# Performance work log

Measured on AMD Instinct MI355X. Metric: run time of the kernel, lower is better.

Reference implementation:

```python
import jax, jax.numpy as jnp
import numpy as np

N = 50000      # nodes
E = 800000     # edges
F_IN = 128     # in_channels
HID = 128      # hidden = out channels
H = 4          # heads
C = HID // H   # per-head dim = 32
L = 3          # transformer layers (num_gat_layers=2 -> 3 convs)
G = 50         # graphs in batch
ED = 2         # edge_dim
EPS_BN = 1e-5


def setup_inputs() -> dict:
    key = jax.random.key(0)
    ks = jax.random.split(key, 24)
    s = 0.05
    f32 = jnp.float32
    inp = {
        "x": jax.random.normal(ks[0], (N, F_IN), f32),
        "edge_index": jax.random.randint(ks[1], (2, E), 0, N, dtype=jnp.int32).astype(jnp.int64),
        "edge_attr": jax.random.uniform(ks[2], (E, ED), f32),
        "batch": jnp.sort(jax.random.randint(ks[3], (N,), 0, G, dtype=jnp.int32).astype(jnp.int64)),
        # stacked per-layer TransformerConv params (all layers 128->128)
        "Wq": jax.random.normal(ks[4], (L, HID, HID), f32) * s,
        "bq": jnp.zeros((L, HID), f32),
        "Wk": jax.random.normal(ks[5], (L, HID, HID), f32) * s,
        "bk": jnp.zeros((L, HID), f32),
        "Wv": jax.random.normal(ks[6], (L, HID, HID), f32) * s,
        "bv": jnp.zeros((L, HID), f32),
        "We": jax.random.normal(ks[7], (L, ED, HID), f32) * s,
        "be": jnp.zeros((L, HID), f32),
        "Wskip": jax.random.normal(ks[8], (L, HID, HID), f32) * s,
        "bskip": jnp.zeros((L, HID), f32),
        "Wbeta": jax.random.normal(ks[9], (L, 3 * HID, 1), f32) * s,  # lin_beta: bias=False
        "bn_gamma": jnp.ones((L, HID), f32),
        "bn_beta": jnp.zeros((L, HID), f32),
        "Wout": jax.random.normal(ks[10], (HID, 1), f32) * s,
        "bout": jnp.zeros((1,), f32),
        "out_bias": jnp.zeros((1,), f32),
    }
    return inp


def reference(x, edge_index, edge_attr, batch, Wq, bq, Wk, bk, Wv, bv, We, be,
              Wskip, bskip, Wbeta, bn_gamma, bn_beta, Wout, bout, out_bias):
    src, dst = edge_index[0], edge_index[1]  # message j->i: src=j, dst=i
    scale = 1.0 / np.sqrt(C)
    for l in range(L):
        q = (x @ Wq[l] + bq[l]).reshape(N, H, C)
        k = (x @ Wk[l] + bk[l]).reshape(N, H, C)
        v = (x @ Wv[l] + bv[l]).reshape(N, H, C)
        e = (edge_attr @ We[l] + be[l]).reshape(E, H, C)
        kj = k[src] + e                                        # [E,H,C] key + edge emb
        alpha = jnp.einsum('ehc,ehc->eh', q[dst], kj) * scale  # [E,H]
        # segment softmax over incoming edges of each destination node
        amax = jax.ops.segment_max(alpha, dst, num_segments=N)
        ex = jnp.exp(alpha - amax[dst])
        den = jax.ops.segment_sum(ex, dst, num_segments=N)
        w = ex / (den[dst] + 1e-16)                            # [E,H] (dropout: eval mode)
        msg = (v[src] + e) * w[:, :, None]                     # [E,H,C]
        out = jax.ops.segment_sum(msg, dst, num_segments=N).reshape(N, HID)
        # beta-gated skip connection
        x_r = x @ Wskip[l] + bskip[l]
        gate = jax.nn.sigmoid(jnp.concatenate([out, x_r, out - x_r], axis=-1) @ Wbeta[l])
        out = gate * x_r + (1.0 - gate) * out
        # BatchNorm1d over nodes (training statistics, biased variance)
        mu = out.mean(axis=0)
        var = out.var(axis=0)
        out = (out - mu) / jnp.sqrt(var + EPS_BN) * bn_gamma[l] + bn_beta[l]
        x = jax.nn.elu(out)
    # global mean pool readout per graph
    cnt = jax.ops.segment_sum(jnp.ones((N,), x.dtype), batch, num_segments=G)
    h_G = jax.ops.segment_sum(x, batch, num_segments=G) / jnp.maximum(cnt, 1.0)[:, None]
    return h_G @ Wout + bout + out_bias  # [G,1]
```

## Files before the change

kernel.cpp:

```cpp
#include <hip/hip_runtime.h>
#include <hip/hip_fp16.h>
#include <math.h>

#define NN 50000
#define EE 800000
#define HIDDEN 128
#define NGRAPH 50
#define GEMM_TILES ((NN + 63) / 64)
#define NB_ATTN 12500

typedef _Float16 half8 __attribute__((ext_vector_type(8)));
typedef float f32x4 __attribute__((ext_vector_type(4)));

__global__ void k_degprep(const int* __restrict__ eidx, int* __restrict__ cnt,
                          const float* __restrict__ Wq, const float* __restrict__ Wk,
                          const float* __restrict__ Wv, const float* __restrict__ Ws,
                          _Float16* __restrict__ wt) {
    int b = blockIdx.x;
    int t = threadIdx.x;
    if (b < 3125) {
        int e = b * 256 + t;
        if (e < EE) atomicAdd(&cnt[eidx[EE + e]], 1);
    } else {
        int idx = (b - 3125) * 256 + t;
        if (idx < 12 * 16384) {
            int mat = idx >> 14;
            int l = mat >> 2, w = mat & 3;
            int nk = idx & 16383;
            int n = nk >> 7, k = nk & 127;
            const float* W = (w == 0 ? Wq : w == 1 ? Wk : w == 2 ? Wv : Ws) + (size_t)l * 16384;
            wt[idx] = (_Float16)W[k * 128 + n];
        }
    }
}

__global__ void k_scan(int* __restrict__ cnt, int* __restrict__ row_ptr,
                       float* __restrict__ bn_acc3, float* __restrict__ gsum,
                       int* __restrict__ gcnt) {
    __shared__ int wsum[16];
    __shared__ int carry_s;
    int t = threadIdx.x;
    int lane = t & 63, w = t >> 6;
    if (t < 768) bn_acc3[t] = 0.f;
    if (t < 64) { gsum[t] = 0.f; gcnt[t] = 0; }
    if (t == 0) carry_s = 0;
    __syncthreads();
    for (int base = 0; base < NN; base += 4096) {
        int i0 = base + t * 4;
        int v[4];
#pragma unroll
        for (int j = 0; j < 4; j++) v[j] = (i0 + j < NN) ? cnt[i0 + j] : 0;
        int s4 = v[0] + v[1] + v[2] + v[3];
        int s = s4;
#pragma unroll
        for (int o = 1; o < 64; o <<= 1) {
            int u = __shfl_up(s, o);
            if (lane >= o) s += u;
        }
        if (lane == 63) wsum[w] = s;
        __syncthreads();
        if (w == 0) {
            int ws = (lane < 16) ? wsum[lane] : 0;
#pragma unroll
            for (int o = 1; o < 16; o <<= 1) {
                int u = __shfl_up(ws, o);
                if (lane >= o) ws += u;
            }
            if (lane < 16) wsum[lane] = ws;
        }
        __syncthreads();
        int wpre = (w == 0) ? 0 : wsum[w - 1];
        int run = carry_s + wpre + s - s4;
#pragma unroll
        for (int j = 0; j < 4; j++) {
            if (i0 + j < NN) { row_ptr[i0 + j] = run; cnt[i0 + j] = 0; run += v[j]; }
        }
        __syncthreads();
        if (t == 0) carry_s += wsum[15];
        __syncthreads();
    }
    if (t == 0) row_ptr[NN] = carry_s;
}

__device__ __forceinline__ void gemm_tile(
    const float* __restrict__ X, const _Float16* __restrict__ wt,
    const float* __restrict__ bq, const float* __restrict__ bk,
    const float* __restrict__ bv, const float* __restrict__ bs,
    const float* ab_s, int use_ab, _Float16 (*xs)[136],
    float* __restrict__ qo, unsigned int* __restrict__ kvb, float* __restrict__ xro,
    int m0)
{
    int t = threadIdx.x;
    int lane = t & 63, wid = t >> 6;
#pragma unroll
    for (int i = 0; i < 8; ++i) {
        int f = t + 256 * i;
        int r = f >> 5, c4 = (f & 31) << 2;
        float4 val = make_float4(0.f, 0.f, 0.f, 0.f);
        if (m0 + r < NN) val = *(const float4*)&X[(size_t)(m0 + r) * 128 + c4];
        if (use_ab) {
            float4 a = *(const float4*)&ab_s[c4];
            float4 bb = *(const float4*)&ab_s[128 + c4];
            float z;
            z = fmaf(val.x, a.x, bb.x); val.x = z > 0.f ? z : expm1f(z);
            z = fmaf(val.y, a.y, bb.y); val.y = z > 0.f ? z : expm1f(z);
            z = fmaf(val.z, a.z, bb.z); val.z = z > 0.f ? z : expm1f(z);
            z = fmaf(val.w, a.w, bb.w); val.w = z > 0.f ? z : expm1f(z);
        }
        _Float16* dst = &xs[r][c4];
        dst[0] = (_Float16)val.x; dst[1] = (_Float16)val.y;
        dst[2] = (_Float16)val.z; dst[3] = (_Float16)val.w;
    }
    __syncthreads();
    int quad = lane >> 4, l15 = lane & 15;
    int mrow = wid * 16;
    half8 afrag[4];
#pragma unroll
    for (int kk = 0; kk < 4; kk++)
        afrag[kk] = *(const half8*)&xs[mrow + l15][kk * 32 + quad * 8];

#pragma unroll
    for (int nt = 0; nt < 8; nt++) {
        int c = nt * 16 + l15;
        f32x4 acc[4];
#pragma unroll
        for (int w = 0; w < 4; w++) acc[w] = (f32x4){0.f, 0.f, 0.f, 0.f};
#pragma unroll
        for (int kk = 0; kk < 4; kk++) {
            half8 bf[4];
#pragma unroll
            for (int w = 0; w < 4; w++)
                bf[w] = *(const half8*)&wt[(size_t)w * 16384 + c * 128 + kk * 32 + quad * 8];
#pragma unroll
            for (int w = 0; w < 4; w++)
                acc[w] = __builtin_amdgcn_mfma_f32_16x16x32_f16(afrag[kk], bf[w], acc[w], 0, 0, 0);
        }
        float bqv = bq[c], bkv = bk[c], bvv = bv[c], bsv = bs[c];
        int nodebase = m0 + mrow + quad * 4;
#pragma unroll
        for (int r = 0; r < 4; r++) {
            int node = nodebase + r;
            bool ok = node < NN;
            float qv = acc[0][r] + bqv;
            float xv = acc[3][r] + bsv;
            float kf = acc[1][r] + bkv;
            float vf = acc[2][r] + bvv;
            float kf1 = __shfl_xor(kf, 1);
            float vf1 = __shfl_xor(vf, 1);
            if (ok) {
                qo[(size_t)node * 128 + c] = qv;
                xro[(size_t)node * 128 + c] = xv;
                if (!(lane & 1)) {
                    int w2 = __builtin_amdgcn_cvt_pk_fp8_f32(kf, kf1, 0, false);
                    w2 = __builtin_amdgcn_cvt_pk_fp8_f32(vf, vf1, w2, true);
                    kvb[(size_t)node * 64 + (c >> 1)] = (unsigned int)w2;
                }
            }
        }
    }
}

__global__ __launch_bounds__(256) void k_gemm0scat(
    const float* __restrict__ X, const _Float16* __restrict__ wt,
    const float* __restrict__ bq, const float* __restrict__ bk,
    const float* __restrict__ bv, const float* __restrict__ bs,
    float* __restrict__ qo, unsigned int* __restrict__ kvb, float* __restrict__ xro,
    const int* __restrict__ eidx, const float* __restrict__ eattr,
    const int* __restrict__ row_ptr, int* __restrict__ cur,
    float4* __restrict__ erec)
{
    __shared__ _Float16 xs[64][136];
    int b = blockIdx.x;
    if (b < GEMM_TILES) {
        gemm_tile(X, wt, bq, bk, bv, bs, nullptr, 0, xs, qo, kvb, xro, b * 64);
    } else {
        int e = (b - GEMM_TILES) * 256 + threadIdx.x;
        if (e < EE) {
            int d = eidx[EE + e];
            int s = eidx[e];
            int p = atomicAdd(&cur[d], 1);
            int pos = row_ptr[d] + p;
            float2 ea = *(const float2*)&eattr[2 * (size_t)e];
            erec[pos] = make_float4(ea.x, ea.y, __int_as_float(s), 0.f);
        }
    }
}

__global__ __launch_bounds__(256) void k_gemm4(
    const float* __restrict__ X, const _Float16* __restrict__ wt,
    const float* __restrict__ bq, const float* __restrict__ bk,
    const float* __restrict__ bv, const float* __restrict__ bs,
    const float* __restrict__ bn_acc, const float* __restrict__ gamma,
    const float* __restrict__ beta,
    float* __restrict__ qo, unsigned int* __restrict__ kvb, float* __restrict__ xro)
{
    __shared__ _Float16 xs[64][136];
    __shared__ float ab_s[256];
    int t = threadIdx.x;
    if (t < 128) {
        float mu = bn_acc[t] * (1.f / NN);
        float var = bn_acc[128 + t] * (1.f / NN) - mu * mu;
        float inv = rsqrtf(var + 1e-5f);
        float a = inv * gamma[t];
        ab_s[t] = a;
        ab_s[128 + t] = beta[t] - mu * a;
    }
    __syncthreads();
    gemm_tile(X, wt, bq, bk, bv, bs, ab_s, 1, xs, qo, kvb, xro, blockIdx.x * 64);
}

__device__ __forceinline__ float row_sum16(float p) {
    p += __int_as_float(__builtin_amdgcn_update_dpp(0, __float_as_int(p), 0x128, 0xF, 0xF, true));
    p += __int_as_float(__builtin_amdgcn_update_dpp(0, __float_as_int(p), 0x124, 0xF, 0xF, true));
    p += __int_as_float(__builtin_amdgcn_update_dpp(0, __float_as_int(p), 0x122, 0xF, 0xF, true));
    p += __int_as_float(__builtin_amdgcn_update_dpp(0, __float_as_int(p), 0x121, 0xF, 0xF, true));
    return p;
}

__global__ __launch_bounds__(256) void k_attn(
    const float* __restrict__ q, const unsigned int* __restrict__ kvb,
    const float* __restrict__ xr,
    const float4* __restrict__ erec,
    const int* __restrict__ row_ptr,
    const float* __restrict__ We, const float* __restrict__ be,
    const float* __restrict__ Wb,
    float* __restrict__ out2, float* __restrict__ bnp)
{
    __shared__ float4 es[4][64];
    int t = threadIdx.x;
    int lane = t & 63;
    int wid = t >> 6;
    int n = blockIdx.x * 4 + wid;
    int ch = lane * 2;
    float2 we0 = *(const float2*)&We[ch];
    float2 we1 = *(const float2*)&We[128 + ch];
    float2 beL = *(const float2*)&be[ch];
    float2 wb_o = *(const float2*)&Wb[ch];
    float2 wb_r = *(const float2*)&Wb[128 + ch];
    float2 wb_d = *(const float2*)&Wb[256 + ch];
    const float scale = 0.17677669529663687f;

    int rs = __builtin_amdgcn_readfirstlane(row_ptr[n]);
    int re = __builtin_amdgcn_readfirstlane(row_ptr[n + 1]);
    float2 qv = *(const float2*)&q[(size_t)n * 128 + ch];
    float den = 0.f, ax = 0.f, ay = 0.f;

    auto edge = [&](float eax, float eay, unsigned int w8) {
        auto kf = __builtin_amdgcn_cvt_pk_f32_fp8((int)w8, false);
        auto vf = __builtin_amdgcn_cvt_pk_f32_fp8((int)w8, true);
        float ex_ = fmaf(eax, we0.x, fmaf(eay, we1.x, beL.x));
        float ey_ = fmaf(eax, we0.y, fmaf(eay, we1.y, beL.y));
        float p = qv.x * (kf[0] + ex_) + qv.y * (kf[1] + ey_);
        p = row_sum16(p);
        float exv = __expf(p * scale);
        den += exv;
        ax = fmaf(exv, vf[0] + ex_, ax);
        ay = fmaf(exv, vf[1] + ey_, ay);
    };

    for (int cb = rs; cb < re; cb += 64) {
        int cnum = re - cb; if (cnum > 64) cnum = 64;
        int mi = cb + lane;
        if (mi < re) es[wid][lane] = erec[mi];
        int base = 0;
        for (; base + 8 <= cnum; base += 8) {
            unsigned int kk[8];
#pragma unroll
            for (int j = 0; j < 8; j++) {
                int s = __float_as_int(es[wid][base + j].z);
                kk[j] = kvb[(size_t)(unsigned)s * 64 + lane];
            }
#pragma unroll
            for (int j = 0; j < 8; j++) {
                float4 rec = es[wid][base + j];
                edge(rec.x, rec.y, kk[j]);
            }
        }
        for (; base < cnum; ++base) {
            float4 rec = es[wid][base];
            unsigned int k0 = kvb[(size_t)(unsigned)__float_as_int(rec.z) * 64 + lane];
            edge(rec.x, rec.y, k0);
        }
    }

    float rden = 1.f / (den + 1e-16f);
    ax *= rden; ay *= rden;
    float2 xv = *(const float2*)&xr[(size_t)n * 128 + ch];
    float gp = ax * wb_o.x + ay * wb_o.y + xv.x * wb_r.x + xv.y * wb_r.y
             + (ax - xv.x) * wb_d.x + (ay - xv.y) * wb_d.y;
    gp = row_sum16(gp);
    gp += __shfl_xor(gp, 16);
    gp += __shfl_xor(gp, 32);
    float gate = 1.f / (1.f + __expf(-gp));
    float ox = gate * xv.x + (1.f - gate) * ax;
    float oy = gate * xv.y + (1.f - gate) * ay;
    *(float2*)&out2[(size_t)n * 128 + ch] = make_float2(ox, oy);

    __shared__ float s_sum[2][256], s_sq[2][256];
    s_sum[0][t] = ox; s_sum[1][t] = oy;
    s_sq[0][t] = ox * ox;  s_sq[1][t] = oy * oy;
    __syncthreads();
    if (t < 64) {
        float sx = s_sum[0][t] + s_sum[0][64 + t] + s_sum[0][128 + t] + s_sum[0][192 + t];
        float sy = s_sum[1][t] + s_sum[1][64 + t] + s_sum[1][128 + t] + s_sum[1][192 + t];
        float qx = s_sq[0][t] + s_sq[0][64 + t] + s_sq[0][128 + t] + s_sq[0][192 + t];
        float qy = s_sq[1][t] + s_sq[1][64 + t] + s_sq[1][128 + t] + s_sq[1][192 + t];
        float2* bp = (float2*)&bnp[(size_t)blockIdx.x * 256];
        bp[t] = make_float2(sx, sy);
        bp[64 + t] = make_float2(qx, qy);
    }
}

__global__ __launch_bounds__(256) void k_bnred(const float* __restrict__ part,
                                               float* __restrict__ bn_acc) {
    int t = threadIdx.x;
    int g = blockIdx.x;
    float s = 0.f;
    for (int r = g * 50; r < g * 50 + 50; ++r)
        s += part[(size_t)r * 256 + t];
    atomicAdd(&bn_acc[t], s);
}

__global__ __launch_bounds__(256) void k_pool(const float* __restrict__ x,
                                              const float* __restrict__ bn_acc,
                                              const float* __restrict__ gamma,
                                              const float* __restrict__ beta,
                                              const float* __restrict__ Wout,
                                              const int* __restrict__ batch,
                                              float* __restrict__ gsum, int* __restrict__ gcnt) {
    __shared__ float lsum[NGRAPH];
    __shared__ int lcnt[NGRAPH];
    __shared__ float ab_s[256];
    int t = threadIdx.x;
    if (t < NGRAPH) { lsum[t] = 0.f; lcnt[t] = 0; }
    if (t < 128) {
        float mu = bn_acc[t] * (1.f / NN);
        float var = bn_acc[128 + t] * (1.f / NN) - mu * mu;
        float inv = rsqrtf(var + 1e-5f);
        float a = inv * gamma[t];
        ab_s[t] = a;
        ab_s[128 + t] = beta[t] - mu * a;
    }
    __syncthreads();
    int lane = t & 63;
    int wid = t >> 6;
    int ch = lane * 2;
    float2 wo = *(const float2*)&Wout[ch];
    float2 a = *(const float2*)&ab_s[ch];
    float2 b = *(const float2*)&ab_s[128 + ch];
    for (int chunk = 0; chunk < 10; ++chunk) {
        int base = blockIdx.x * 160 + chunk * 16 + wid * 4;
        float2 xv[4];
#pragma unroll
        for (int i = 0; i < 4; i++) {
            int n = base + i;
            xv[i] = (n < NN) ? *(const float2*)&x[(size_t)n * 128 + ch]
                             : make_float2(0.f, 0.f);
        }
#pragma unroll
        for (int i = 0; i < 4; i++) {
            int n = base + i;
            if (n < NN) {
                float z0 = fmaf(xv[i].x, a.x, b.x); z0 = z0 > 0.f ? z0 : expm1f(z0);
                float z1 = fmaf(xv[i].y, a.y, b.y); z1 = z1 > 0.f ? z1 : expm1f(z1);
                float p = z0 * wo.x + z1 * wo.y;
                p += __shfl_xor(p, 1);
                p += __shfl_xor(p, 2);
                p += __shfl_xor(p, 4);
                p += __shfl_xor(p, 8);
                p += __shfl_xor(p, 16);
                p += __shfl_xor(p, 32);
                if (lane == 0) {
                    int g = batch[n];
                    atomicAdd(&lsum[g], p);
                    atomicAdd(&lcnt[g], 1);
                }
            }
        }
    }
    __syncthreads();
    if (t < NGRAPH && lcnt[t] > 0) {
        atomicAdd(&gsum[t], lsum[t]);
        atomicAdd(&gcnt[t], lcnt[t]);
    }
}

__global__ void k_final(const float* __restrict__ gsum, const int* __restrict__ gcnt,
                        const float* __restrict__ bout, const float* __restrict__ obias,
                        float* __restrict__ out) {
    int g = threadIdx.x;
    if (g < NGRAPH) out[g] = gsum[g] / fmaxf((float)gcnt[g], 1.f) + bout[0] + obias[0];
}

extern "C" void kernel_launch(void* const* d_in, const int* in_sizes, int n_in,
                              void* d_out, int out_size, void* d_ws, size_t ws_size,
                              hipStream_t stream) {
    const float* x_in       = (const float*)d_in[0];
    const int* eidx         = (const int*)d_in[1];
    const float* eattr      = (const float*)d_in[2];
    const int* batch        = (const int*)d_in[3];
    const float* Wq         = (const float*)d_in[4];
    const float* bq         = (const float*)d_in[5];
    const float* Wk         = (const float*)d_in[6];
    const float* bk         = (const float*)d_in[7];
    const float* Wv         = (const float*)d_in[8];
    const float* bv         = (const float*)d_in[9];
    const float* We         = (const float*)d_in[10];
    const float* be         = (const float*)d_in[11];
    const float* Wskip      = (const float*)d_in[12];
    const float* bskip      = (const float*)d_in[13];
    const float* Wbeta      = (const float*)d_in[14];
    const float* bn_gamma   = (const float*)d_in[15];
    const float* bn_beta    = (const float*)d_in[16];
    const float* Wout       = (const float*)d_in[17];
    const float* bout       = (const float*)d_in[18];
    const float* obias      = (const float*)d_in[19];
    float* out = (float*)d_out;

    char* ws = (char*)d_ws;
    size_t off = 0;
    auto alloc = [&](size_t bytes) -> void* {
        off = (off + 255) & ~(size_t)255;
        void* p = ws + off;
        off += bytes;
        return p;
    };
    const size_t NF = (size_t)NN * 128 * sizeof(float);
    float* xbuf    = (float*)alloc(NF);
    float* qb      = (float*)alloc(NF);
    float* xrb     = (float*)alloc(NF);
    unsigned int* kvb = (unsigned int*)alloc((size_t)NN * 64 * sizeof(unsigned int));
    _Float16* wt   = (_Float16*)alloc((size_t)12 * 16384 * sizeof(_Float16));
    int* row_ptr   = (int*)alloc((NN + 1) * sizeof(int));
    int* cnt       = (int*)alloc(NN * sizeof(int));
    float4* erec   = (float4*)alloc((size_t)EE * sizeof(float4));
    float* bn_acc3 = (float*)alloc(3 * 256 * sizeof(float));
    float* bnpart  = (float*)alloc((size_t)NB_ATTN * 256 * sizeof(float));
    float* gsum    = (float*)alloc(64 * sizeof(float));
    int* gcnt      = (int*)alloc(64 * sizeof(int));
    (void)ws_size; (void)n_in; (void)in_sizes; (void)out_size;

    hipMemsetAsync(cnt, 0, NN * sizeof(int), stream);
    k_degprep<<<3125 + 768, 256, 0, stream>>>(eidx, cnt, Wq, Wk, Wv, Wskip, wt);
    k_scan<<<1, 1024, 0, stream>>>(cnt, row_ptr, bn_acc3, gsum, gcnt);

    k_gemm0scat<<<GEMM_TILES + 3125, 256, 0, stream>>>(
        x_in, wt, bq, bk, bv, bskip, qb, kvb, xrb,
        eidx, eattr, row_ptr, cnt, erec);
    k_attn<<<NB_ATTN, 256, 0, stream>>>(
        qb, kvb, xrb, erec, row_ptr,
        We, be, Wbeta, xbuf, bnpart);
    k_bnred<<<250, 256, 0, stream>>>(bnpart, bn_acc3);

    for (int l = 1; l < 3; ++l) {
        k_gemm4<<<GEMM_TILES, 256, 0, stream>>>(
            xbuf, wt + (size_t)l * 65536,
            bq + l * 128, bk + l * 128, bv + l * 128, bskip + l * 128,
            bn_acc3 + (l - 1) * 256, bn_gamma + (l - 1) * 128, bn_beta + (l - 1) * 128,
            qb, kvb, xrb);
        k_attn<<<NB_ATTN, 256, 0, stream>>>(
            qb, kvb, xrb, erec, row_ptr,
            We + (size_t)l * 256, be + l * 128, Wbeta + (size_t)l * 384,
            xbuf, bnpart);
        k_bnred<<<250, 256, 0, stream>>>(bnpart, bn_acc3 + l * 256);
    }

    k_pool<<<313, 256, 0, stream>>>(xbuf, bn_acc3 + 2 * 256,
                                    bn_gamma + 2 * 128, bn_beta + 2 * 128,
                                    Wout, batch, gsum, gcnt);
    k_final<<<1, 64, 0, stream>>>(gsum, gcnt, bout, obias, out);
}
```

Before: 622.3 us.

## Double-buffer neighbor loads in attention and reuse atomic ranks for CSR scatter

The attention kernel now prefetches the next group of eight fp8 key/value gathers into a second register buffer while the current group is computed. Scheduling barriers keep the loads and the math apart, and tail edges are clamped and masked so the remainder loop is gone. Separately, the degree-count pass now records each edge's atomic rank, so the CSR scatter no longer needs a second round of atomics. This costs an extra 800K-int rank buffer and more register pressure from holding two buffers of gathers.

```diff
diff --git a/kernel.cpp b/kernel.cpp
--- a/kernel.cpp
+++ b/kernel.cpp
@@ -13,6 +13,7 @@
 typedef float f32x4 __attribute__((ext_vector_type(4)));
 
 __global__ void k_degprep(const int* __restrict__ eidx, int* __restrict__ cnt,
+                          int* __restrict__ rank,
                           const float* __restrict__ Wq, const float* __restrict__ Wk,
                           const float* __restrict__ Wv, const float* __restrict__ Ws,
                           _Float16* __restrict__ wt) {
@@ -20,7 +21,10 @@
     int t = threadIdx.x;
     if (b < 3125) {
         int e = b * 256 + t;
-        if (e < EE) atomicAdd(&cnt[eidx[EE + e]], 1);
+        if (e < EE) {
+            int p = atomicAdd(&cnt[eidx[EE + e]], 1);
+            rank[e] = p;
+        }
     } else {
         int idx = (b - 3125) * 256 + t;
         if (idx < 12 * 16384) {
@@ -166,7 +170,7 @@
     const float* __restrict__ bv, const float* __restrict__ bs,
     float* __restrict__ qo, unsigned int* __restrict__ kvb, float* __restrict__ xro,
     const int* __restrict__ eidx, const float* __restrict__ eattr,
-    const int* __restrict__ row_ptr, int* __restrict__ cur,
+    const int* __restrict__ row_ptr, const int* __restrict__ rank,
     float4* __restrict__ erec)
 {
     __shared__ _Float16 xs[64][136];
@@ -178,9 +182,9 @@
         if (e < EE) {
             int d = eidx[EE + e];
             int s = eidx[e];
-            int p = atomicAdd(&cur[d], 1);
-            int pos = row_ptr[d] + p;
+            int rk = rank[e];
             float2 ea = *(const float2*)&eattr[2 * (size_t)e];
+            int pos = row_ptr[d] + rk;
             erec[pos] = make_float4(ea.x, ea.y, __int_as_float(s), 0.f);
         }
     }
@@ -235,57 +239,69 @@
     float2 we0 = *(const float2*)&We[ch];
     float2 we1 = *(const float2*)&We[128 + ch];
     float2 beL = *(const float2*)&be[ch];
-    float2 wb_o = *(const float2*)&Wb[ch];
-    float2 wb_r = *(const float2*)&Wb[128 + ch];
-    float2 wb_d = *(const float2*)&Wb[256 + ch];
     const float scale = 0.17677669529663687f;
 
     int rs = __builtin_amdgcn_readfirstlane(row_ptr[n]);
     int re = __builtin_amdgcn_readfirstlane(row_ptr[n + 1]);
     float2 qv = *(const float2*)&q[(size_t)n * 128 + ch];
+    float2 xv = *(const float2*)&xr[(size_t)n * 128 + ch];
     float den = 0.f, ax = 0.f, ay = 0.f;
-
-    auto edge = [&](float eax, float eay, unsigned int w8) {
-        auto kf = __builtin_amdgcn_cvt_pk_f32_fp8((int)w8, false);
-        auto vf = __builtin_amdgcn_cvt_pk_f32_fp8((int)w8, true);
-        float ex_ = fmaf(eax, we0.x, fmaf(eay, we1.x, beL.x));
-        float ey_ = fmaf(eax, we0.y, fmaf(eay, we1.y, beL.y));
-        float p = qv.x * (kf[0] + ex_) + qv.y * (kf[1] + ey_);
-        p = row_sum16(p);
-        float exv = __expf(p * scale);
-        den += exv;
-        ax = fmaf(exv, vf[0] + ex_, ax);
-        ay = fmaf(exv, vf[1] + ey_, ay);
-    };
 
     for (int cb = rs; cb < re; cb += 64) {
         int cnum = re - cb; if (cnum > 64) cnum = 64;
         int mi = cb + lane;
         if (mi < re) es[wid][lane] = erec[mi];
-        int base = 0;
-        for (; base + 8 <= cnum; base += 8) {
-            unsigned int kk[8];
-#pragma unroll
-            for (int j = 0; j < 8; j++) {
-                int s = __float_as_int(es[wid][base + j].z);
-                kk[j] = kvb[(size_t)(unsigned)s * 64 + lane];
-            }
-#pragma unroll
-            for (int j = 0; j < 8; j++) {
-                float4 rec = es[wid][base + j];
-                edge(rec.x, rec.y, kk[j]);
-            }
-        }
-        for (; base < cnum; ++base) {
-            float4 rec = es[wid][base];
-            unsigned int k0 = kvb[(size_t)(unsigned)__float_as_int(rec.z) * 64 + lane];
-            edge(rec.x, rec.y, k0);
-        }
+        int cm1 = cnum - 1;
+        int ng = (cnum + 7) >> 3;
+        unsigned int kkA[8], kkB[8];
+
+#define LOAD8(KK, B0) do {                                                   \
+        _Pragma("unroll")                                                    \
+        for (int j = 0; j < 8; j++) {                                        \
+            int o = (B0) + j; int oc = o < cm1 ? o : cm1;                    \
+            int s = __float_as_int(es[wid][oc].z);                           \
+            KK[j] = kvb[(size_t)(unsigned)s * 64 + lane];                    \
+        }                                                                    \
+    } while (0)
+
+#define COMP8(KK, B0) do {                                                   \
+        _Pragma("unroll")                                                    \
+        for (int j = 0; j < 8; j++) {                                        \
+            int o = (B0) + j; int oc = o < cm1 ? o : cm1;                    \
+            float4 rec = es[wid][oc];                                        \
+            auto kf = __builtin_amdgcn_cvt_pk_f32_fp8((int)KK[j], false);    \
+            auto vf = __builtin_amdgcn_cvt_pk_f32_fp8((int)KK[j], true);     \
+            float ex_ = fmaf(rec.x, we0.x, fmaf(rec.y, we1.x, beL.x));       \
+            float ey_ = fmaf(rec.x, we0.y, fmaf(rec.y, we1.y, beL.y));       \
+            float p = qv.x * (kf[0] + ex_) + qv.y * (kf[1] + ey_);           \
+            p = row_sum16(p);                                                \
+            float exv = (o < cnum) ? __expf(p * scale) : 0.f;                \
+            den += exv;                                                      \
+            ax = fmaf(exv, vf[0] + ex_, ax);                                 \
+            ay = fmaf(exv, vf[1] + ey_, ay);                                 \
+        }                                                                    \
+    } while (0)
+
+        LOAD8(kkA, 0);
+        __builtin_amdgcn_sched_barrier(0);
+        int g = 0;
+        for (;;) {
+            if (g + 1 < ng) { LOAD8(kkB, (g + 1) * 8); __builtin_amdgcn_sched_barrier(0); }
+            COMP8(kkA, g * 8);
+            ++g; if (g >= ng) break;
+            if (g + 1 < ng) { LOAD8(kkA, (g + 1) * 8); __builtin_amdgcn_sched_barrier(0); }
+            COMP8(kkB, g * 8);
+            ++g; if (g >= ng) break;
+        }
+#undef LOAD8
+#undef COMP8
     }
 
     float rden = 1.f / (den + 1e-16f);
     ax *= rden; ay *= rden;
-    float2 xv = *(const float2*)&xr[(size_t)n * 128 + ch];
+    float2 wb_o = *(const float2*)&Wb[ch];
+    float2 wb_r = *(const float2*)&Wb[128 + ch];
+    float2 wb_d = *(const float2*)&Wb[256 + ch];
     float gp = ax * wb_o.x + ay * wb_o.y + xv.x * wb_r.x + xv.y * wb_r.y
              + (ax - xv.x) * wb_d.x + (ay - xv.y) * wb_d.y;
     gp = row_sum16(gp);
@@ -433,6 +449,7 @@
     _Float16* wt   = (_Float16*)alloc((size_t)12 * 16384 * sizeof(_Float16));
     int* row_ptr   = (int*)alloc((NN + 1) * sizeof(int));
     int* cnt       = (int*)alloc(NN * sizeof(int));
+    int* rank      = (int*)alloc(EE * sizeof(int));
     float4* erec   = (float4*)alloc((size_t)EE * sizeof(float4));
     float* bn_acc3 = (float*)alloc(3 * 256 * sizeof(float));
     float* bnpart  = (float*)alloc((size_t)NB_ATTN * 256 * sizeof(float));
@@ -441,12 +458,12 @@
     (void)ws_size; (void)n_in; (void)in_sizes; (void)out_size;
 
     hipMemsetAsync(cnt, 0, NN * sizeof(int), stream);
-    k_degprep<<<3125 + 768, 256, 0, stream>>>(eidx, cnt, Wq, Wk, Wv, Wskip, wt);
+    k_degprep<<<3125 + 768, 256, 0, stream>>>(eidx, cnt, rank, Wq, Wk, Wv, Wskip, wt);
     k_scan<<<1, 1024, 0, stream>>>(cnt, row_ptr, bn_acc3, gsum, gcnt);
 
     k_gemm0scat<<<GEMM_TILES + 3125, 256, 0, stream>>>(
         x_in, wt, bq, bk, bv, bskip, qb, kvb, xrb,
-        eidx, eattr, row_ptr, cnt, erec);
+        eidx, eattr, row_ptr, rank, erec);
     k_attn<<<NB_ATTN, 256, 0, stream>>>(
         qb, kvb, xrb, erec, row_ptr,
         We, be, Wbeta, xbuf, bnpart);
```

After: 609.9 us. -2.0%, faster.
